# Kernel tuning notes

Measured on AMD Instinct MI355X. Metric: run time of the kernel, lower is better.

## Reference

```python
import jax, jax.numpy as jnp
import numpy as np

NUM_HEADS = 8
MAX_REL = 32  # max_relative_positions
LN_EPS = 1e-5


def _conv1x1(x, W, b):
    # x: (B, C, H, W), W: (Cout, Cin), b: (Cout,)
    return jnp.einsum('bchw,oc->bohw', x, W) + b[None, :, None, None]


def setup_inputs() -> dict:
    key = jax.random.key(0)
    ks = jax.random.split(key, 10)
    B, C, H, W = 2, 512, 48, 48
    L = H * W
    s = 1.0 / np.sqrt(C)
    inp = {
        'x': jax.random.normal(ks[0], (B, C, H, W), jnp.float32),
        'mask': jax.random.randint(ks[1], (1, NUM_HEADS, L, L), 0, 2).astype(bool),
        'learnable_pos': jax.random.normal(ks[2], (1, C, H, W), jnp.float32) * 0.02,
        'Wq': jax.random.normal(ks[3], (C, C), jnp.float32) * s,
        'bq': jnp.zeros((C,), jnp.float32),
        'Wk': jax.random.normal(ks[4], (C, C), jnp.float32) * s,
        'bk': jnp.zeros((C,), jnp.float32),
        'Wv': jax.random.normal(ks[5], (C, C), jnp.float32) * s,
        'bv': jnp.zeros((C,), jnp.float32),
        'Wo': jax.random.normal(ks[6], (C, C), jnp.float32) * s,
        'bo': jnp.zeros((C,), jnp.float32),
        'rel_table': jax.random.normal(ks[7], (NUM_HEADS, 2 * MAX_REL + 1), jnp.float32) * 0.02,
        'ln_gamma': jnp.ones((C,), jnp.float32),
        'ln_beta': jnp.zeros((C,), jnp.float32),
    }
    return inp


def reference(x, mask, learnable_pos, Wq, bq, Wk, bk, Wv, bv, Wo, bo,
              rel_table, ln_gamma, ln_beta):
    B, C, H, W = x.shape
    L = H * W
    hd = C // NUM_HEADS
    residual = x

    xp = x + learnable_pos
    q = _conv1x1(xp, Wq, bq)
    k = _conv1x1(xp, Wk, bk)
    v = _conv1x1(xp, Wv, bv)

    def split_heads(t):  # (B,C,H,W) -> (B, heads, L, hd)
        return t.reshape(B, NUM_HEADS, hd, L).transpose(0, 1, 3, 2)

    q, k, v = split_heads(q), split_heads(k), split_heads(v)

    scale = 1.0 / np.sqrt(hd).astype(np.float32)
    scores = jnp.einsum('bhld,bhmd->bhlm', q, k) * scale  # (B,H,L,L)

    # relative positional bias per head
    pos = jnp.arange(L)
    rp = jnp.clip(pos[:, None] - pos[None, :], -MAX_REL, MAX_REL) + MAX_REL  # (L,L)
    scores = scores + rel_table[:, rp][None]  # (1,heads,L,L) broadcast

    scores = jnp.where(mask, scores, jnp.float32(-1e9))
    attn = jax.nn.softmax(scores, axis=-1)

    out = jnp.einsum('bhlm,bhmd->bhld', attn, v)  # (B,heads,L,hd)
    out = out.transpose(0, 1, 3, 2).reshape(B, C, H, W)
    out = _conv1x1(out, Wo, bo)

    y = residual + out
    # LayerNorm over channels (channels-last permute in original)
    yl = y.transpose(0, 2, 3, 1)  # (B,H,W,C)
    mu = jnp.mean(yl, axis=-1, keepdims=True)
    var = jnp.var(yl, axis=-1, keepdims=True)
    yl = (yl - mu) * jax.lax.rsqrt(var + LN_EPS) * ln_gamma + ln_beta
    return yl.transpose(0, 3, 1, 2)
```

## Files before the change

### kernel.cpp

```cpp
#include <hip/hip_runtime.h>
#include <cstdint>

#define L_SEQ 2304
#define CDIM  512
#define NHEADS 8
#define HD    64
#define LL    ((size_t)L_SEQ * L_SEQ)
#define ROWS_TOT (16 * L_SEQ)
#define PERBL ((size_t)2 * L_SEQ * 512)

typedef short  s8v  __attribute__((ext_vector_type(8)));
typedef float  f4v  __attribute__((ext_vector_type(4)));

__device__ __forceinline__ ushort f2bf(float f) {
    union { float f; uint32_t u; } v; v.f = f;
    uint32_t u = v.u;
    uint32_t r = (u + 0x7FFFu + ((u >> 16) & 1u)) >> 16;
    return (ushort)r;
}

__device__ __forceinline__ float bf2f(ushort u) {
    union { uint32_t u; float f; } v; v.u = (uint32_t)u << 16;
    return v.f;
}

__global__ __launch_bounds__(256) void prep_w(
    const float* __restrict__ Wq, const float* __restrict__ Wk,
    const float* __restrict__ Wv, const float* __restrict__ Wo,
    ushort* __restrict__ wb)
{
    const int i   = blockIdx.x * 256 + threadIdx.x;
    const int mat = i >> 16;
    const int j   = i & 65535;
    const float* src = (mat == 0) ? Wq : (mat == 1) ? Wk : (mat == 2) ? Wv : Wo;
    const float4 w = ((const float4*)src)[j];
    ushort4 o;
    o.x = f2bf(w.x); o.y = f2bf(w.y); o.z = f2bf(w.z); o.w = f2bf(w.w);
    ((ushort4*)(wb + (size_t)mat * 262144))[j] = o;
}

__global__ __launch_bounds__(256) void xpose(
    const float* __restrict__ x, const float* __restrict__ pos,
    ushort* __restrict__ xt)
{
    __shared__ ushort T[64][72];
    const int l0 = blockIdx.x * 64;
    const int c0 = blockIdx.y * 64;
    const int b  = blockIdx.z;
    const int t  = threadIdx.x;
    const int cc = t >> 2;
    const int l4 = (t & 3) * 16;
    const size_t off  = ((size_t)b * CDIM + c0 + cc) * L_SEQ + l0 + l4;
    const size_t poff = (size_t)(c0 + cc) * L_SEQ + l0 + l4;
    #pragma unroll
    for (int j4 = 0; j4 < 4; j4++) {
        const float4 xv = *(const float4*)&x[off + j4 * 4];
        const float4 pv = *(const float4*)&pos[poff + j4 * 4];
        T[cc][l4 + j4 * 4 + 0] = f2bf(xv.x + pv.x);
        T[cc][l4 + j4 * 4 + 1] = f2bf(xv.y + pv.y);
        T[cc][l4 + j4 * 4 + 2] = f2bf(xv.z + pv.z);
        T[cc][l4 + j4 * 4 + 3] = f2bf(xv.w + pv.w);
    }
    __syncthreads();
    const int lr = t >> 2;
    const int c4 = (t & 3) * 16;
    ushort o[16];
    #pragma unroll
    for (int j = 0; j < 16; j++) o[j] = T[c4 + j][lr];
    ushort* dst = &xt[((size_t)b * L_SEQ + l0 + lr) * 512 + c0 + c4];
    *(ushort4*)&dst[0]  = *(ushort4*)&o[0];
    *(ushort4*)&dst[4]  = *(ushort4*)&o[4];
    *(ushort4*)&dst[8]  = *(ushort4*)&o[8];
    *(ushort4*)&dst[12] = *(ushort4*)&o[12];
}

__global__ __launch_bounds__(256) void qkv_mfma(
    const ushort* __restrict__ xt, const ushort* __restrict__ wb,
    const float* __restrict__ bq, const float* __restrict__ bk,
    const float* __restrict__ bv,
    ushort* __restrict__ q_t, ushort* __restrict__ k_t, ushort* __restrict__ v_t)
{
    __shared__ __align__(16) ushort Bs[3][1024 * 8];
    const int l0  = blockIdx.x * 64;
    const int o0  = blockIdx.y * 64;
    const int b   = blockIdx.z;
    const int t = threadIdx.x, w = t >> 6, lane = t & 63;
    const int n16 = lane & 15, q4 = lane >> 4;

    const ushort* A = xt + ((size_t)b * L_SEQ + l0 + w * 16 + n16) * 512 + q4 * 8;

    s8v areg[16];
    #pragma unroll
    for (int i = 0; i < 16; i++) areg[i] = *(const s8v*)&A[i * 32];

    int sOff[4];
    #pragma unroll
    for (int i = 0; i < 4; i++) {
        const int c  = t + 256 * i;
        const int fr = c >> 6, ln = c & 63;
        sOff[i] = (o0 + (fr & 3) * 16 + (ln & 15)) * 512 + (fr >> 2) * 32 + (ln >> 4) * 8;
    }

    s8v breg[3][4];
    #pragma unroll
    for (int m = 0; m < 3; m++)
        #pragma unroll
        for (int i = 0; i < 4; i++)
            breg[m][i] = *(const s8v*)&wb[(size_t)m * 262144 + sOff[i]];

    f4v acc[3][4] = {};
    for (int kb = 0; kb < 512; kb += 128) {
        __syncthreads();
        #pragma unroll
        for (int m = 0; m < 3; m++)
            #pragma unroll
            for (int i = 0; i < 4; i++)
                *(s8v*)&Bs[m][(t + 256 * i) * 8] = breg[m][i];
        __syncthreads();
        if (kb < 384) {
            #pragma unroll
            for (int m = 0; m < 3; m++)
                #pragma unroll
                for (int i = 0; i < 4; i++)
                    breg[m][i] = *(const s8v*)&wb[(size_t)m * 262144 + sOff[i] + kb + 128];
        }
        #pragma unroll
        for (int ks = 0; ks < 4; ks++) {
            const s8v a = areg[(kb >> 5) + ks];
            #pragma unroll
            for (int m = 0; m < 3; m++)
                #pragma unroll
                for (int t4 = 0; t4 < 4; t4++) {
                    const s8v bf = *(const s8v*)&Bs[m][((ks * 4 + t4) * 64 + lane) * 8];
                    acc[m][t4] = __builtin_amdgcn_mfma_f32_16x16x32_bf16(a, bf, acc[m][t4], 0, 0, 0);
                }
        }
    }

    const int h = o0 >> 6;
    const int rowbase = l0 + w * 16 + q4 * 4;

    #pragma unroll
    for (int m = 0; m < 2; m++) {
        const float* bias = (m == 0) ? bq : bk;
        const float sc = (m == 0) ? 0.125f : 1.0f;
        ushort* op = (m == 0 ? q_t : k_t) + ((size_t)(b * NHEADS + h)) * L_SEQ * HD;
        #pragma unroll
        for (int t4 = 0; t4 < 4; t4++) {
            const float bi = bias[o0 + t4 * 16 + n16];
            #pragma unroll
            for (int r = 0; r < 4; r++)
                op[(size_t)(rowbase + r) * HD + t4 * 16 + n16] = f2bf((acc[m][t4][r] + bi) * sc);
        }
    }
    {
        ushort* op = v_t + ((size_t)(b * NHEADS + h)) * HD * L_SEQ;
        #pragma unroll
        for (int t4 = 0; t4 < 4; t4++) {
            const float bi = bv[o0 + t4 * 16 + n16];
            ushort4 st;
            st.x = f2bf(acc[2][t4][0] + bi);
            st.y = f2bf(acc[2][t4][1] + bi);
            st.z = f2bf(acc[2][t4][2] + bi);
            st.w = f2bf(acc[2][t4][3] + bi);
            *(ushort4*)&op[(size_t)(t4 * 16 + n16) * L_SEQ + rowbase] = st;
        }
    }
}

__global__ __launch_bounds__(256) void flash_attn_mfma(
    const ushort* __restrict__ q, const ushort* __restrict__ k,
    const ushort* __restrict__ vt, const int* __restrict__ mask,
    const float* __restrict__ rel_table, ushort* __restrict__ Opart,
    float* __restrict__ Mpart, float* __restrict__ Lpart)
{
    __shared__ __align__(16) ushort Kf[512 * 8];
    __shared__ __align__(16) ushort Vf[512 * 8];
    __shared__ __align__(16) ushort Pb[4 * 16 * 72];
    __shared__ float rt[65];

    const int t    = threadIdx.x;
    const int id   = blockIdx.x;
    const int h    = id & 7;
    const int s2   = id >> 3;
    const int b    = s2 & 1;
    const int half = (s2 >> 1) & 1;
    const int qb   = s2 >> 2;
    const int bh   = b * NHEADS + h;
    const int l0   = qb * 64;
    const int w    = t >> 6;
    const int lane = t & 63;
    const int n16  = lane & 15;
    const int q4   = lane >> 4;

    if (t < 65) rt[t] = rel_table[h * 65 + t];

    const ushort* qp = q  + (size_t)bh * L_SEQ * HD;
    const ushort* kp = k  + (size_t)bh * L_SEQ * HD;
    const ushort* vp = vt + (size_t)bh * HD * L_SEQ;
    const int*    mp = mask + (size_t)h * LL;

    const int qrow = l0 + w * 16 + n16;
    const s8v qA0 = *(const s8v*)&qp[(size_t)qrow * HD + q4 * 8];
    const s8v qA1 = *(const s8v*)&qp[(size_t)qrow * HD + 32 + q4 * 8];

    f4v O[4] = {{0.f,0.f,0.f,0.f},{0.f,0.f,0.f,0.f},{0.f,0.f,0.f,0.f},{0.f,0.f,0.f,0.f}};
    float mrun[4] = {-3e38f, -3e38f, -3e38f, -3e38f};
    float lrun[4] = {0.f, 0.f, 0.f, 0.f};

    int sT[2], sS[2], sQ[2], sN[2];
    #pragma unroll
    for (int cc = 0; cc < 2; cc++) {
        const int c = t + cc * 256;
        const int g = c >> 6;
        sT[cc] = g >> 1; sS[cc] = g & 1;
        sQ[cc] = (c >> 4) & 3; sN[cc] = c & 15;
    }

    const int rowbase = l0 + w * 16 + q4 * 4;
    const int kbase = half * 1152;

    for (int mt = 0; mt < 18; mt++) {
        const int mb = kbase + mt * 64;
        __syncthreads();
        #pragma unroll
        for (int cc = 0; cc < 2; cc++) {
            const int c = t + cc * 256;
            const int key = sT[cc] * 16 + sN[cc];
            const int d0  = sS[cc] * 32 + sQ[cc] * 8;
            *(s8v*)&Kf[c * 8] = *(const s8v*)&kp[(size_t)(mb + key) * HD + d0];
            const int dd = sT[cc] * 16 + sN[cc];
            *(s8v*)&Vf[c * 8] = *(const s8v*)&vp[(size_t)dd * L_SEQ + mb + d0];
        }
        __syncthreads();

        int mreg[4][4];
        #pragma unroll
        for (int t4 = 0; t4 < 4; t4++)
            #pragma unroll
            for (int r = 0; r < 4; r++)
                mreg[t4][r] = mp[(size_t)(rowbase + r) * L_SEQ + mb + t4 * 16 + n16];

        f4v S[4];
        #pragma unroll
        for (int t4 = 0; t4 < 4; t4++) {
            const s8v b0 = *(const s8v*)&Kf[((t4 * 2 + 0) * 64 + lane) * 8];
            const s8v b1 = *(const s8v*)&Kf[((t4 * 2 + 1) * 64 + lane) * 8];
            f4v acc = {0.f, 0.f, 0.f, 0.f};
            acc = __builtin_amdgcn_mfma_f32_16x16x32_bf16(qA0, b0, acc, 0, 0, 0);
            acc = __builtin_amdgcn_mfma_f32_16x16x32_bf16(qA1, b1, acc, 0, 0, 0);
            S[t4] = acc;
        }

        #pragma unroll
        for (int t4 = 0; t4 < 4; t4++) {
            const int A = (l0 + w * 16) - (mb + t4 * 16);
            if (A >= 47) {
                const float bu = rt[64];
                #pragma unroll
                for (int r = 0; r < 4; r++) S[t4][r] += bu;
            } else if (A <= -47) {
                const float bu = rt[0];
                #pragma unroll
                for (int r = 0; r < 4; r++) S[t4][r] += bu;
            } else {
                #pragma unroll
                for (int r = 0; r < 4; r++) {
                    int dix = A + q4 * 4 + r - n16;
                    dix = min(max(dix, -32), 32) + 32;
                    S[t4][r] += rt[dix];
                }
            }
            #pragma unroll
            for (int r = 0; r < 4; r++)
                if (mreg[t4][r] == 0) S[t4][r] = -1e9f;
        }

        float mx[4];
        #pragma unroll
        for (int r = 0; r < 4; r++) {
            float m0 = fmaxf(fmaxf(S[0][r], S[1][r]), fmaxf(S[2][r], S[3][r]));
            m0 = fmaxf(m0, __shfl_xor(m0, 1));
            m0 = fmaxf(m0, __shfl_xor(m0, 2));
            m0 = fmaxf(m0, __shfl_xor(m0, 4));
            m0 = fmaxf(m0, __shfl_xor(m0, 8));
            mx[r] = m0;
        }
        float al[4];
        #pragma unroll
        for (int r = 0; r < 4; r++) {
            const float mn = fmaxf(mrun[r], mx[r]);
            al[r] = __expf(mrun[r] - mn);
            mrun[r] = mn;
            float sum = 0.f;
            #pragma unroll
            for (int t4 = 0; t4 < 4; t4++) {
                const float p = __expf(S[t4][r] - mn);
                S[t4][r] = p;
                sum += p;
                Pb[w * 1152 + (q4 * 4 + r) * 72 + t4 * 16 + n16] = f2bf(p);
            }
            sum += __shfl_xor(sum, 1);
            sum += __shfl_xor(sum, 2);
            sum += __shfl_xor(sum, 4);
            sum += __shfl_xor(sum, 8);
            lrun[r] = lrun[r] * al[r] + sum;
        }

        const s8v pf0 = *(const s8v*)&Pb[w * 1152 + n16 * 72 + q4 * 8];
        const s8v pf1 = *(const s8v*)&Pb[w * 1152 + n16 * 72 + 32 + q4 * 8];
        #pragma unroll
        for (int t4 = 0; t4 < 4; t4++) {
            f4v o = O[t4];
            #pragma unroll
            for (int r = 0; r < 4; r++) o[r] *= al[r];
            const s8v v0 = *(const s8v*)&Vf[((t4 * 2 + 0) * 64 + lane) * 8];
            const s8v v1 = *(const s8v*)&Vf[((t4 * 2 + 1) * 64 + lane) * 8];
            o = __builtin_amdgcn_mfma_f32_16x16x32_bf16(pf0, v0, o, 0, 0, 0);
            o = __builtin_amdgcn_mfma_f32_16x16x32_bf16(pf1, v1, o, 0, 0, 0);
            O[t4] = o;
        }
    }

    ushort* op = Opart + (size_t)half * PERBL + (size_t)b * L_SEQ * 512;
    #pragma unroll
    for (int r = 0; r < 4; r++) {
        const size_t base = (size_t)(rowbase + r) * 512 + h * 64;
        #pragma unroll
        for (int t4 = 0; t4 < 4; t4++)
            op[base + t4 * 16 + n16] = f2bf(O[t4][r]);
    }
    if (n16 == 0) {
        const size_t sb = (size_t)half * ROWS_TOT + (size_t)bh * L_SEQ;
        #pragma unroll
        for (int r = 0; r < 4; r++) {
            Mpart[sb + rowbase + r] = mrun[r];
            Lpart[sb + rowbase + r] = lrun[r];
        }
    }
}

__global__ __launch_bounds__(256) void combine_kernel(
    const ushort* __restrict__ O01, const float* __restrict__ Mp,
    const float* __restrict__ Lp, ushort* __restrict__ at)
{
    const int i   = blockIdx.x * 256 + threadIdx.x;
    const int c8  = i & 63;
    const int row = i >> 6;
    const int b   = row / L_SEQ;
    const int l   = row - b * L_SEQ;
    const int h   = c8 >> 3;
    const size_t s = (size_t)(b * NHEADS + h) * L_SEQ + l;
    const float m0 = Mp[s], m1 = Mp[ROWS_TOT + s];
    const float l0 = Lp[s], l1 = Lp[ROWS_TOT + s];
    const float M  = fmaxf(m0, m1);
    const float w0 = __expf(m0 - M);
    const float w1 = __expf(m1 - M);
    const float inv = 1.0f / (l0 * w0 + l1 * w1);
    const float f0 = w0 * inv;
    const float f1 = w1 * inv;
    const size_t o = (size_t)row * 512 + c8 * 8;
    const ushort4 a0 = *(const ushort4*)&O01[o];
    const ushort4 a1 = *(const ushort4*)&O01[o + 4];
    const ushort4 c0 = *(const ushort4*)&O01[PERBL + o];
    const ushort4 c1 = *(const ushort4*)&O01[PERBL + o + 4];
    ushort4 r0, r1;
    r0.x = f2bf(bf2f(a0.x) * f0 + bf2f(c0.x) * f1);
    r0.y = f2bf(bf2f(a0.y) * f0 + bf2f(c0.y) * f1);
    r0.z = f2bf(bf2f(a0.z) * f0 + bf2f(c0.z) * f1);
    r0.w = f2bf(bf2f(a0.w) * f0 + bf2f(c0.w) * f1);
    r1.x = f2bf(bf2f(a1.x) * f0 + bf2f(c1.x) * f1);
    r1.y = f2bf(bf2f(a1.y) * f0 + bf2f(c1.y) * f1);
    r1.z = f2bf(bf2f(a1.z) * f0 + bf2f(c1.z) * f1);
    r1.w = f2bf(bf2f(a1.w) * f0 + bf2f(c1.w) * f1);
    *(ushort4*)&at[o]     = r0;
    *(ushort4*)&at[o + 4] = r1;
}

__global__ __launch_bounds__(256) void out_mfma(
    const ushort* __restrict__ at, const ushort* __restrict__ wb,
    const float* __restrict__ bo, const float* __restrict__ x,
    float* __restrict__ y)
{
    __shared__ __align__(16) ushort Bs[1024 * 8];
    const int l0 = blockIdx.x * 64;
    const int o0 = blockIdx.y * 64;
    const int b  = blockIdx.z;
    const int t = threadIdx.x, w = t >> 6, lane = t & 63;
    const int n16 = lane & 15, q4 = lane >> 4;

    const ushort* A = at + ((size_t)b * L_SEQ + l0 + w * 16 + n16) * 512 + q4 * 8;
    const ushort* W = wb + (size_t)3 * 262144;

    s8v areg[16];
    #pragma unroll
    for (int i = 0; i < 16; i++) areg[i] = *(const s8v*)&A[i * 32];

    int sOff[4];
    #pragma unroll
    for (int i = 0; i < 4; i++) {
        const int c  = t + 256 * i;
        const int fr = c >> 6, ln = c & 63;
        sOff[i] = (o0 + (fr & 3) * 16 + (ln & 15)) * 512 + (fr >> 2) * 32 + (ln >> 4) * 8;
    }

    s8v breg[4];
    #pragma unroll
    for (int i = 0; i < 4; i++) breg[i] = *(const s8v*)&W[sOff[i]];

    f4v acc[4] = {{0.f,0.f,0.f,0.f},{0.f,0.f,0.f,0.f},{0.f,0.f,0.f,0.f},{0.f,0.f,0.f,0.f}};
    for (int kb = 0; kb < 512; kb += 128) {
        __syncthreads();
        #pragma unroll
        for (int i = 0; i < 4; i++)
            *(s8v*)&Bs[(t + 256 * i) * 8] = breg[i];
        __syncthreads();
        if (kb < 384) {
            #pragma unroll
            for (int i = 0; i < 4; i++)
                breg[i] = *(const s8v*)&W[sOff[i] + kb + 128];
        }
        #pragma unroll
        for (int ks = 0; ks < 4; ks++) {
            const s8v a = areg[(kb >> 5) + ks];
            #pragma unroll
            for (int t4 = 0; t4 < 4; t4++) {
                const s8v bf = *(const s8v*)&Bs[((ks * 4 + t4) * 64 + lane) * 8];
                acc[t4] = __builtin_amdgcn_mfma_f32_16x16x32_bf16(a, bf, acc[t4], 0, 0, 0);
            }
        }
    }

    const int rowbase = l0 + w * 16 + q4 * 4;
    #pragma unroll
    for (int t4 = 0; t4 < 4; t4++) {
        const int o = o0 + t4 * 16 + n16;
        const float bi = bo[o];
        const size_t off = ((size_t)b * CDIM + o) * L_SEQ + rowbase;
        const float4 xv = *(const float4*)&x[off];
        float4 st;
        st.x = acc[t4][0] + bi + xv.x;
        st.y = acc[t4][1] + bi + xv.y;
        st.z = acc[t4][2] + bi + xv.z;
        st.w = acc[t4][3] + bi + xv.w;
        *(float4*)&y[off] = st;
    }
}

__global__ __launch_bounds__(256) void ln_kernel(
    float* __restrict__ y, const float* __restrict__ gamma,
    const float* __restrict__ beta)
{
    const int t = threadIdx.x;
    const int p = t & 31;
    const int g = t >> 5;
    const int pos = blockIdx.x * 32 + p;
    const int b = (pos >= L_SEQ) ? 1 : 0;
    const int l = pos - b * L_SEQ;
    float* col = y + (size_t)b * CDIM * L_SEQ + l;

    float s = 0.f, sq = 0.f;
    for (int c = g * 64; c < g * 64 + 64; c++) {
        const float v = col[(size_t)c * L_SEQ];
        s += v; sq += v * v;
    }
    __shared__ float S1[8][32];
    __shared__ float S2[8][32];
    S1[g][p] = s; S2[g][p] = sq;
    __syncthreads();
    if (t < 32) {
        float ss = 0.f, qq = 0.f;
        #pragma unroll
        for (int gg = 0; gg < 8; gg++) { ss += S1[gg][t]; qq += S2[gg][t]; }
        const float mu = ss * (1.0f / CDIM);
        const float var = qq * (1.0f / CDIM) - mu * mu;
        S1[0][t] = mu;
        S2[0][t] = rsqrtf(var + 1e-5f);
    }
    __syncthreads();
    const float mu = S1[0][p];
    const float rs = S2[0][p];
    for (int c = g * 64; c < g * 64 + 64; c++) {
        const float v = col[(size_t)c * L_SEQ];
        col[(size_t)c * L_SEQ] = (v - mu) * rs * gamma[c] + beta[c];
    }
}

extern "C" void kernel_launch(void* const* d_in, const int* in_sizes, int n_in,
                              void* d_out, int out_size, void* d_ws, size_t ws_size,
                              hipStream_t stream) {
    const float* x    = (const float*)d_in[0];
    const int* mask   = (const int*)d_in[1];
    const float* pos  = (const float*)d_in[2];
    const float* Wq   = (const float*)d_in[3];
    const float* bq   = (const float*)d_in[4];
    const float* Wk   = (const float*)d_in[5];
    const float* bk   = (const float*)d_in[6];
    const float* Wv   = (const float*)d_in[7];
    const float* bv   = (const float*)d_in[8];
    const float* Wo   = (const float*)d_in[9];
    const float* bo   = (const float*)d_in[10];
    const float* rel  = (const float*)d_in[11];
    const float* gam  = (const float*)d_in[12];
    const float* bet  = (const float*)d_in[13];

    ushort* qw  = (ushort*)d_ws;
    ushort* kw  = qw + PERBL;
    ushort* vw  = kw + PERBL;
    ushort* xtw = vw + PERBL;
    ushort* wbw = xtw + PERBL;
    ushort* Opart = wbw + (size_t)4 * 512 * 512;
    float* Mpart = (float*)(Opart + 2 * PERBL);
    float* Lpart = Mpart + 2 * ROWS_TOT;
    ushort* attnT = xtw;
    float* y = (float*)d_out;

    prep_w<<<dim3(1024), 256, 0, stream>>>(Wq, Wk, Wv, Wo, wbw);

    xpose<<<dim3(L_SEQ / 64, CDIM / 64, 2), 256, 0, stream>>>(x, pos, xtw);

    qkv_mfma<<<dim3(L_SEQ / 64, CDIM / 64, 2), 256, 0, stream>>>(
        xtw, wbw, bq, bk, bv, qw, kw, vw);

    flash_attn_mfma<<<dim3(1152), 256, 0, stream>>>(qw, kw, vw, mask, rel,
                                                    Opart, Mpart, Lpart);

    combine_kernel<<<dim3(1152), 256, 0, stream>>>(Opart, Mpart, Lpart, attnT);

    out_mfma<<<dim3(L_SEQ / 64, CDIM / 64, 2), 256, 0, stream>>>(
        attnT, wbw, bo, x, y);

    ln_kernel<<<(2 * L_SEQ) / 32, 256, 0, stream>>>(y, gam, bet);
}
```

Baseline: 394.9 us.

## Pack attention mask into bitmasks and drop split-K attention with combine

Adds a pre-pass that packs the int mask into 64-bit ballot words per row and key block, so the attention kernel reads one word per row instead of sixteen ints per lane. The attention kernel no longer splits the key range in two; each block walks all 36 key tiles and normalizes its output directly, which removes the partial-output buffers and the combine kernel. The catch is that the attention grid halves to 576 blocks, which may lower occupancy, and the packing pass still reads the full mask once.

```diff
diff --git a/kernel.cpp b/kernel.cpp
--- a/kernel.cpp
+++ b/kernel.cpp
@@ -6,7 +6,7 @@
 #define NHEADS 8
 #define HD    64
 #define LL    ((size_t)L_SEQ * L_SEQ)
-#define ROWS_TOT (16 * L_SEQ)
+#define NKB   36
 #define PERBL ((size_t)2 * L_SEQ * 512)
 
 typedef short  s8v  __attribute__((ext_vector_type(8)));
@@ -37,6 +37,23 @@
     ushort4 o;
     o.x = f2bf(w.x); o.y = f2bf(w.y); o.z = f2bf(w.z); o.w = f2bf(w.w);
     ((ushort4*)(wb + (size_t)mat * 262144))[j] = o;
+}
+
+__global__ __launch_bounds__(256) void pack_mask(
+    const int* __restrict__ mask, unsigned long long* __restrict__ mpk)
+{
+    const int t    = threadIdx.x;
+    const int w    = t >> 6;
+    const int lane = t & 63;
+    const int base = blockIdx.x * 64 + w * 16;
+    for (int it = 0; it < 16; it++) {
+        const int g   = base + it;
+        const int row = g / NKB;
+        const int kb  = g - row * NKB;
+        const unsigned long long bits =
+            __ballot(mask[(size_t)row * L_SEQ + kb * 64 + lane] != 0);
+        if (lane == 0) mpk[g] = bits;
+    }
 }
 
 __global__ __launch_bounds__(256) void xpose(
@@ -170,9 +187,8 @@
 
 __global__ __launch_bounds__(256) void flash_attn_mfma(
     const ushort* __restrict__ q, const ushort* __restrict__ k,
-    const ushort* __restrict__ vt, const int* __restrict__ mask,
-    const float* __restrict__ rel_table, ushort* __restrict__ Opart,
-    float* __restrict__ Mpart, float* __restrict__ Lpart)
+    const ushort* __restrict__ vt, const unsigned long long* __restrict__ mpk,
+    const float* __restrict__ rel_table, ushort* __restrict__ attnT)
 {
     __shared__ __align__(16) ushort Kf[512 * 8];
     __shared__ __align__(16) ushort Vf[512 * 8];
@@ -182,10 +198,9 @@
     const int t    = threadIdx.x;
     const int id   = blockIdx.x;
     const int h    = id & 7;
-    const int s2   = id >> 3;
-    const int b    = s2 & 1;
-    const int half = (s2 >> 1) & 1;
-    const int qb   = s2 >> 2;
+    const int slot = id >> 3;
+    const int b    = slot & 1;
+    const int qb   = slot >> 1;
     const int bh   = b * NHEADS + h;
     const int l0   = qb * 64;
     const int w    = t >> 6;
@@ -198,7 +213,7 @@
     const ushort* qp = q  + (size_t)bh * L_SEQ * HD;
     const ushort* kp = k  + (size_t)bh * L_SEQ * HD;
     const ushort* vp = vt + (size_t)bh * HD * L_SEQ;
-    const int*    mp = mask + (size_t)h * LL;
+    const unsigned long long* mh = mpk + (size_t)h * L_SEQ * NKB;
 
     const int qrow = l0 + w * 16 + n16;
     const s8v qA0 = *(const s8v*)&qp[(size_t)qrow * HD + q4 * 8];
@@ -218,10 +233,9 @@
     }
 
     const int rowbase = l0 + w * 16 + q4 * 4;
-    const int kbase = half * 1152;
-
-    for (int mt = 0; mt < 18; mt++) {
-        const int mb = kbase + mt * 64;
+
+    for (int mt = 0; mt < 36; mt++) {
+        const int mb = mt * 64;
         __syncthreads();
         #pragma unroll
         for (int cc = 0; cc < 2; cc++) {
@@ -234,12 +248,10 @@
         }
         __syncthreads();
 
-        int mreg[4][4];
-        #pragma unroll
-        for (int t4 = 0; t4 < 4; t4++)
-            #pragma unroll
-            for (int r = 0; r < 4; r++)
-                mreg[t4][r] = mp[(size_t)(rowbase + r) * L_SEQ + mb + t4 * 16 + n16];
+        unsigned long long mk[4];
+        #pragma unroll
+        for (int r = 0; r < 4; r++)
+            mk[r] = mh[(size_t)(rowbase + r) * NKB + mt];
 
         f4v S[4];
         #pragma unroll
@@ -271,9 +283,10 @@
                     S[t4][r] += rt[dix];
                 }
             }
+            const int bp = t4 * 16 + n16;
             #pragma unroll
             for (int r = 0; r < 4; r++)
-                if (mreg[t4][r] == 0) S[t4][r] = -1e9f;
+                if (((mk[r] >> bp) & 1ull) == 0) S[t4][r] = -1e9f;
         }
 
         float mx[4];
@@ -322,59 +335,17 @@
         }
     }
 
-    ushort* op = Opart + (size_t)half * PERBL + (size_t)b * L_SEQ * 512;
+    float inv[4];
+    #pragma unroll
+    for (int r = 0; r < 4; r++) inv[r] = 1.0f / lrun[r];
+    ushort* op = attnT + (size_t)b * L_SEQ * 512;
     #pragma unroll
     for (int r = 0; r < 4; r++) {
         const size_t base = (size_t)(rowbase + r) * 512 + h * 64;
         #pragma unroll
         for (int t4 = 0; t4 < 4; t4++)
-            op[base + t4 * 16 + n16] = f2bf(O[t4][r]);
-    }
-    if (n16 == 0) {
-        const size_t sb = (size_t)half * ROWS_TOT + (size_t)bh * L_SEQ;
-        #pragma unroll
-        for (int r = 0; r < 4; r++) {
-            Mpart[sb + rowbase + r] = mrun[r];
-            Lpart[sb + rowbase + r] = lrun[r];
-        }
-    }
-}
-
-__global__ __launch_bounds__(256) void combine_kernel(
-    const ushort* __restrict__ O01, const float* __restrict__ Mp,
-    const float* __restrict__ Lp, ushort* __restrict__ at)
-{
-    const int i   = blockIdx.x * 256 + threadIdx.x;
-    const int c8  = i & 63;
-    const int row = i >> 6;
-    const int b   = row / L_SEQ;
-    const int l   = row - b * L_SEQ;
-    const int h   = c8 >> 3;
-    const size_t s = (size_t)(b * NHEADS + h) * L_SEQ + l;
-    const float m0 = Mp[s], m1 = Mp[ROWS_TOT + s];
-    const float l0 = Lp[s], l1 = Lp[ROWS_TOT + s];
-    const float M  = fmaxf(m0, m1);
-    const float w0 = __expf(m0 - M);
-    const float w1 = __expf(m1 - M);
-    const float inv = 1.0f / (l0 * w0 + l1 * w1);
-    const float f0 = w0 * inv;
-    const float f1 = w1 * inv;
-    const size_t o = (size_t)row * 512 + c8 * 8;
-    const ushort4 a0 = *(const ushort4*)&O01[o];
-    const ushort4 a1 = *(const ushort4*)&O01[o + 4];
-    const ushort4 c0 = *(const ushort4*)&O01[PERBL + o];
-    const ushort4 c1 = *(const ushort4*)&O01[PERBL + o + 4];
-    ushort4 r0, r1;
-    r0.x = f2bf(bf2f(a0.x) * f0 + bf2f(c0.x) * f1);
-    r0.y = f2bf(bf2f(a0.y) * f0 + bf2f(c0.y) * f1);
-    r0.z = f2bf(bf2f(a0.z) * f0 + bf2f(c0.z) * f1);
-    r0.w = f2bf(bf2f(a0.w) * f0 + bf2f(c0.w) * f1);
-    r1.x = f2bf(bf2f(a1.x) * f0 + bf2f(c1.x) * f1);
-    r1.y = f2bf(bf2f(a1.y) * f0 + bf2f(c1.y) * f1);
-    r1.z = f2bf(bf2f(a1.z) * f0 + bf2f(c1.z) * f1);
-    r1.w = f2bf(bf2f(a1.w) * f0 + bf2f(c1.w) * f1);
-    *(ushort4*)&at[o]     = r0;
-    *(ushort4*)&at[o + 4] = r1;
+            op[base + t4 * 16 + n16] = f2bf(O[t4][r] * inv[r]);
+    }
 }
 
 __global__ __launch_bounds__(256) void out_mfma(
@@ -509,23 +480,20 @@
     ushort* vw  = kw + PERBL;
     ushort* xtw = vw + PERBL;
     ushort* wbw = xtw + PERBL;
-    ushort* Opart = wbw + (size_t)4 * 512 * 512;
-    float* Mpart = (float*)(Opart + 2 * PERBL);
-    float* Lpart = Mpart + 2 * ROWS_TOT;
+    unsigned long long* mpk = (unsigned long long*)(wbw + (size_t)4 * 262144);
     ushort* attnT = xtw;
     float* y = (float*)d_out;
 
     prep_w<<<dim3(1024), 256, 0, stream>>>(Wq, Wk, Wv, Wo, wbw);
 
+    pack_mask<<<dim3(10368), 256, 0, stream>>>(mask, mpk);
+
     xpose<<<dim3(L_SEQ / 64, CDIM / 64, 2), 256, 0, stream>>>(x, pos, xtw);
 
     qkv_mfma<<<dim3(L_SEQ / 64, CDIM / 64, 2), 256, 0, stream>>>(
         xtw, wbw, bq, bk, bv, qw, kw, vw);
 
-    flash_attn_mfma<<<dim3(1152), 256, 0, stream>>>(qw, kw, vw, mask, rel,
-                                                    Opart, Mpart, Lpart);
-
-    combine_kernel<<<dim3(1152), 256, 0, stream>>>(Opart, Mpart, Lpart, attnT);
+    flash_attn_mfma<<<dim3(576), 256, 0, stream>>>(qw, kw, vw, mpk, rel, attnT);
 
     out_mfma<<<dim3(L_SEQ / 64, CDIM / 64, 2), 256, 0, stream>>>(
         attnT, wbw, bo, x, y);
```

Result: slower. 462.8 us (+17.2%).
